# Kernel optimization log

Hardware: AMD Instinct MI355X
Metric: run time of the kernel (lower is better)

## Reference

```python
import jax, jax.numpy as jnp
import numpy as np

N_NODES = 100000
N_EDGES = 400000
IN_DIM, HID, OUT_DIM, NUM_REL = 768, 256, 128, 3


def _init_linear(key, fan_in, fan_out):
    k1, k2 = jax.random.split(key)
    s = 1.0 / np.sqrt(fan_in)
    W = jax.random.uniform(k1, (fan_in, fan_out), jnp.float32, -s, s)
    b = jax.random.uniform(k2, (fan_out,), jnp.float32, -s, s)
    return W, b


def setup_inputs() -> dict:
    key = jax.random.key(0)
    ks = jax.random.split(key, 12)
    x = jax.random.normal(ks[0], (N_NODES, IN_DIM), jnp.float32)
    edge_index = jax.random.randint(ks[1], (2, N_EDGES), 0, N_NODES, jnp.int64 if jax.config.jax_enable_x64 else jnp.int32).astype(jnp.int32)
    edge_type = jax.random.randint(ks[2], (N_EDGES,), 0, NUM_REL).astype(jnp.int32)
    W1, b1 = _init_linear(ks[3], IN_DIM, HID)
    s = 1.0 / np.sqrt(HID)
    conv1_W = jax.random.uniform(ks[4], (NUM_REL, HID, HID), jnp.float32, -s, s)
    conv1_root = jax.random.uniform(ks[5], (HID, HID), jnp.float32, -s, s)
    conv1_bias = jnp.zeros((HID,), jnp.float32)
    conv2_W = jax.random.uniform(ks[6], (NUM_REL, HID, HID), jnp.float32, -s, s)
    conv2_root = jax.random.uniform(ks[7], (HID, HID), jnp.float32, -s, s)
    conv2_bias = jnp.zeros((HID,), jnp.float32)
    W2, b2 = _init_linear(ks[8], HID, OUT_DIM)
    Wc, bc = _init_linear(ks[9], OUT_DIM, 2)
    return {"x": x, "edge_index": edge_index, "edge_type": edge_type,
            "batch_size": 1024,
            "W1": W1, "b1": b1,
            "conv1_W": conv1_W, "conv1_root": conv1_root, "conv1_bias": conv1_bias,
            "conv2_W": conv2_W, "conv2_root": conv2_root, "conv2_bias": conv2_bias,
            "W2": W2, "b2": b2, "Wc": Wc, "bc": bc}


def rgcn_conv(h, src, dst, edge_type, W, root, bias):
    # PyG RGCNConv: mean aggregation per relation + root transform + bias
    n = h.shape[0]
    hs = h[src]                                   # [E, HID] gather
    out = h @ root + bias                         # root/self term
    for r in range(NUM_REL):                      # fixed small relation count
        w = (edge_type == r).astype(h.dtype)      # [E]
        msg = (hs @ W[r]) * w[:, None]            # per-relation transform
        ssum = jax.ops.segment_sum(msg, dst, num_segments=n)
        cnt = jax.ops.segment_sum(w, dst, num_segments=n)
        out = out + ssum / jnp.maximum(cnt, 1.0)[:, None]
    return out


def reference(x, edge_index, edge_type, batch_size,
              W1, b1, conv1_W, conv1_root, conv1_bias,
              conv2_W, conv2_root, conv2_bias, W2, b2, Wc, bc):
    src, dst = edge_index[0], edge_index[1]
    h = jax.nn.relu(x @ W1 + b1)                  # linear1 + ReLU
    h = rgcn_conv(h, src, dst, edge_type, conv1_W, conv1_root, conv1_bias)
    # dropout: identity at inference
    h = rgcn_conv(h, src, dst, edge_type, conv2_W, conv2_root, conv2_bias)
    h = jax.nn.relu(h @ W2 + b2)                  # linear2 + ReLU
    logits = h @ Wc + bc                          # classifier
    return logits[:batch_size]
```

## Files before the change

kernel.cpp:

```cpp
#include <hip/hip_runtime.h>


#define N_NODES 100000
#define N_EDGES 400000
#define IN_DIM  768
#define HID     256
#define OUT_DIM 128
#define NREL    3
#define BATCH   1024
#define KCAT    1024
#define MSGW    768
#define CAP0    32768
#define CAP1    8192
#define ECAP1   32768
#define ECAP2   8192
#define NBAR    12

typedef __attribute__((ext_vector_type(8))) short bf16x8;
typedef __attribute__((ext_vector_type(4))) float f32x4;

static __device__ __forceinline__ int imin(int a, int b) { return a < b ? a : b; }

static __device__ __forceinline__ unsigned short f2bf(float f) {
    union { float f; unsigned int u; } v; v.f = f;
    unsigned int r = v.u + 0x7FFFu + ((v.u >> 16) & 1u);
    return (unsigned short)(r >> 16);
}

struct Prm {
    const float* x; const int* ei; const int* et;
    const float *W1, *b1, *c1W, *c1root, *c1bias, *c2W, *c2root, *c2bias, *W2, *b2, *Wc, *bc;
    float* out;
    uint4* zp; int nz;
    int* bar;
    int *need1, *need0, *map1, *map0, *idx1, *idx0, *elist1, *elist2;
    int *n1ctr, *n0ctr, *ectr1, *ectr2;
    float *cnt1, *cnt2, *Amsg1, *Amsg2, *h0c, *h1c, *h2;
    unsigned short *w1s, *B1s, *B2s;
};

static __device__ __forceinline__ void gbar(int* bar, int slot) {
    __syncthreads();
    if (threadIdx.x == 0) {
        int* c = bar + slot * 16;
        __threadfence();
        atomicAdd(c, 1);
        int nb = (int)gridDim.x;
        long spins = 0;
        while (__hip_atomic_load(c, __ATOMIC_ACQUIRE, __HIP_MEMORY_SCOPE_AGENT) < nb) {
            __builtin_amdgcn_s_sleep(2);
            if (++spins > (1L << 24)) break;
        }
        __threadfence();
    }
    __syncthreads();
}


static __device__ void weight_prep_dev(const Prm& p, int gtid, int gstr) {
    const int P1n = (IN_DIM * HID) / 8, P2n = (KCAT * HID) / 8;
    for (int u = gtid; u < P1n + 2 * P2n; u += gstr) {
        unsigned int pk[4];
        if (u < P1n) {
            int base = u * 8;
            int j0 = base & 31, c = (base >> 5) & 255, s = base >> 13;
            #pragma unroll
            for (int q = 0; q < 4; q++) {
                unsigned short lo = f2bf(p.W1[((s * 32 + j0 + 2 * q) << 8) + c]);
                unsigned short hi = f2bf(p.W1[((s * 32 + j0 + 2 * q + 1) << 8) + c]);
                pk[q] = (unsigned int)lo | ((unsigned int)hi << 16);
            }
            *(uint4*)&p.w1s[base] = make_uint4(pk[0], pk[1], pk[2], pk[3]);
        } else {
            int which2 = (u - P1n) >= P2n;
            const float* root = which2 ? p.c2root : p.c1root;
            const float* Wr   = which2 ? p.c2W : p.c1W;
            unsigned short* dst = which2 ? p.B2s : p.B1s;
            int base = ((u - P1n) - (which2 ? P2n : 0)) * 8;
            int j0 = base & 31, c = (base >> 5) & 255, s = base >> 13;
            int k0 = s * 32 + j0;
            #pragma unroll
            for (int q = 0; q < 4; q++) {
                int ka = k0 + 2 * q, kb = ka + 1;
                float va = (ka < HID) ? root[(ka << 8) + c] : Wr[((ka - HID) << 8) + c];
                float vb = (kb < HID) ? root[(kb << 8) + c] : Wr[((kb - HID) << 8) + c];
                pk[q] = (unsigned int)f2bf(va) | ((unsigned int)f2bf(vb) << 16);
            }
            *(uint4*)&dst[base] = make_uint4(pk[0], pk[1], pk[2], pk[3]);
        }
    }
}

static __device__ void scatter_dev(const int* __restrict__ ei, const int* __restrict__ et,
                                   const int* __restrict__ elist, const int* __restrict__ ectr, int ecap,
                                   const int* __restrict__ mapSrc, const int* __restrict__ mapDst,
                                   const float* __restrict__ hsrc,
                                   float* __restrict__ Amsg, float* __restrict__ cnt,
                                   int cntStride, int gtid, int gstr) {
    int n = imin(*ectr, ecap);
    int tot = n * 64;
    for (int g = gtid; g < tot; g += gstr) {
        int ii = g >> 6, lane = g & 63;
        int e = elist[ii];
        int d = ei[N_EDGES + e];
        int row = mapDst ? mapDst[d] : d;
        if (row < 0) continue;
        int s = mapSrc[ei[e]];
        if (s < 0) continue;
        int r = et[e];
        float4 v = *(const float4*)(hsrc + (size_t)s * HID + lane * 4);
        float* dp = Amsg + (size_t)row * MSGW + (size_t)r * HID + lane * 4;
        atomicAdd(dp + 0, v.x);
        atomicAdd(dp + 1, v.y);
        atomicAdd(dp + 2, v.z);
        atomicAdd(dp + 3, v.w);
        if (lane == 0) atomicAdd(cnt + (size_t)r * cntStride + row, 1.0f);
    }
}

static __device__ void gemm1_tile(const float* __restrict__ x, const int* __restrict__ idx0,
                                  const unsigned short* __restrict__ w1s, const float* __restrict__ b1,
                                  float* __restrict__ h0c, int bm, int M,
                                  unsigned short (*As)[40], unsigned short (*Bs)[40]) {
    int tid = threadIdx.x;
    int w = tid >> 6, lane = tid & 63;
    int l16 = lane & 15, lhi = lane >> 4;
    int ar = tid >> 2, ac = tid & 3;
    int gr = idx0[imin(bm + ar, M - 1)];
    const float* aptr = x + (size_t)gr * IN_DIM + ac * 8;

    f32x4 acc[16];
    #pragma unroll
    for (int i = 0; i < 16; i++) acc[i] = (f32x4)0.0f;

    for (int k0 = 0; k0 < IN_DIM; k0 += 32) {
        float4 a0 = *(const float4*)(aptr + k0);
        float4 a1 = *(const float4*)(aptr + k0 + 4);
        unsigned int p0 = (unsigned int)f2bf(a0.x) | ((unsigned int)f2bf(a0.y) << 16);
        unsigned int p1 = (unsigned int)f2bf(a0.z) | ((unsigned int)f2bf(a0.w) << 16);
        unsigned int p2 = (unsigned int)f2bf(a1.x) | ((unsigned int)f2bf(a1.y) << 16);
        unsigned int p3 = (unsigned int)f2bf(a1.z) | ((unsigned int)f2bf(a1.w) << 16);
        *(uint4*)&As[ar][ac * 8] = make_uint4(p0, p1, p2, p3);

        const uint4* bsrc = (const uint4*)(w1s + ((size_t)(k0 >> 5) * 256 + tid) * 32);
        int bswz = (tid >> 3) & 3;
        uint4 b0 = bsrc[0], b1v = bsrc[1], b2 = bsrc[2], b3 = bsrc[3];
        *(uint4*)&Bs[tid][(0 ^ bswz) * 8] = b0;
        *(uint4*)&Bs[tid][(1 ^ bswz) * 8] = b1v;
        *(uint4*)&Bs[tid][(2 ^ bswz) * 8] = b2;
        *(uint4*)&Bs[tid][(3 ^ bswz) * 8] = b3;
        __syncthreads();

        bf16x8 af = *(bf16x8*)&As[w * 16 + l16][lhi * 8];
        #pragma unroll
        for (int f = 0; f < 16; f++) {
            int col = f * 16 + l16;
            bf16x8 bf = *(bf16x8*)&Bs[col][(lhi ^ ((col >> 3) & 3)) * 8];
            acc[f] = __builtin_amdgcn_mfma_f32_16x16x32_bf16(af, bf, acc[f], 0, 0, 0);
        }
        __syncthreads();
    }

    #pragma unroll
    for (int f = 0; f < 16; f++) {
        int col = f * 16 + l16;
        float bb = b1[col];
        #pragma unroll
        for (int reg = 0; reg < 4; reg++) {
            int row = bm + w * 16 + lhi * 4 + reg;
            if (row < M) h0c[(size_t)row * HID + col] = fmaxf(acc[f][reg] + bb, 0.0f);
        }
    }
}

static __device__ void conv_tile(const float* __restrict__ hsrc,
                                 const int* __restrict__ idx, const int* __restrict__ map,
                                 const float* __restrict__ Amsg,
                                 const float* __restrict__ cnt, int cntStride,
                                 const unsigned short* __restrict__ Bt, const float* __restrict__ bias,
                                 float* __restrict__ Cout, int bm, int M,
                                 unsigned short (*As)[40], unsigned short (*Bs)[40]) {
    int tid = threadIdx.x;
    int w = tid >> 6, lane = tid & 63;
    int l16 = lane & 15, lhi = lane >> 4;
    int ar = tid >> 2, ac = tid & 3;
    int row = imin(bm + ar, M - 1);
    int node = idx ? idx[row] : row;
    int grow = map[node]; if (grow < 0) grow = 0;
    const float* rootp = hsrc + (size_t)grow * HID + ac * 8;
    const float* msgp  = Amsg + (size_t)row * MSGW + ac * 8;
    float sc[NREL];
    #pragma unroll
    for (int r = 0; r < NREL; r++)
        sc[r] = 1.0f / fmaxf(cnt[(size_t)r * cntStride + row], 1.0f);

    f32x4 acc[16];
    #pragma unroll
    for (int i = 0; i < 16; i++) acc[i] = (f32x4)0.0f;

    for (int k0 = 0; k0 < KCAT; k0 += 32) {
        float4 a0, a1;
        if (k0 < HID) {
            a0 = *(const float4*)(rootp + k0);
            a1 = *(const float4*)(rootp + k0 + 4);
        } else {
            float s = sc[(k0 - HID) >> 8];
            a0 = *(const float4*)(msgp + (k0 - HID));
            a1 = *(const float4*)(msgp + (k0 - HID) + 4);
            a0.x *= s; a0.y *= s; a0.z *= s; a0.w *= s;
            a1.x *= s; a1.y *= s; a1.z *= s; a1.w *= s;
        }
        unsigned int p0 = (unsigned int)f2bf(a0.x) | ((unsigned int)f2bf(a0.y) << 16);
        unsigned int p1 = (unsigned int)f2bf(a0.z) | ((unsigned int)f2bf(a0.w) << 16);
        unsigned int p2 = (unsigned int)f2bf(a1.x) | ((unsigned int)f2bf(a1.y) << 16);
        unsigned int p3 = (unsigned int)f2bf(a1.z) | ((unsigned int)f2bf(a1.w) << 16);
        *(uint4*)&As[ar][ac * 8] = make_uint4(p0, p1, p2, p3);

        const uint4* bsrc = (const uint4*)(Bt + ((size_t)(k0 >> 5) * 256 + tid) * 32);
        int bswz = (tid >> 3) & 3;
        uint4 b0 = bsrc[0], b1v = bsrc[1], b2 = bsrc[2], b3 = bsrc[3];
        *(uint4*)&Bs[tid][(0 ^ bswz) * 8] = b0;
        *(uint4*)&Bs[tid][(1 ^ bswz) * 8] = b1v;
        *(uint4*)&Bs[tid][(2 ^ bswz) * 8] = b2;
        *(uint4*)&Bs[tid][(3 ^ bswz) * 8] = b3;
        __syncthreads();

        bf16x8 af = *(bf16x8*)&As[w * 16 + l16][lhi * 8];
        #pragma unroll
        for (int f = 0; f < 16; f++) {
            int col = f * 16 + l16;
            bf16x8 bf = *(bf16x8*)&Bs[col][(lhi ^ ((col >> 3) & 3)) * 8];
            acc[f] = __builtin_amdgcn_mfma_f32_16x16x32_bf16(af, bf, acc[f], 0, 0, 0);
        }
        __syncthreads();
    }

    #pragma unroll
    for (int f = 0; f < 16; f++) {
        int col = f * 16 + l16;
        float bb = bias[col];
        #pragma unroll
        for (int reg = 0; reg < 4; reg++) {
            int r = bm + w * 16 + lhi * 4 + reg;
            if (r < M) Cout[(size_t)r * HID + col] = acc[f][reg] + bb;
        }
    }
}

static __device__ void lin2_tile(const float* __restrict__ h2, const float* __restrict__ W2,
                                 const float* __restrict__ b2, const float* __restrict__ Wc,
                                 const float* __restrict__ bc, float* __restrict__ out, int bm,
                                 float (*Asf)[36], float (*Bsf)[132]) {
    int tid = threadIdx.x;
    int tx = tid & 15, ty = tid >> 4;
    int brow = tid >> 4, bch = tid & 15;

    float acc[2][8] = {};

    for (int k0 = 0; k0 < HID; k0 += 16) {
        if (tid < 128) {
            int arow = tid >> 2, ach = tid & 3;
            float4 av = *(const float4*)(h2 + (size_t)(bm + arow) * HID + k0 + ach * 4);
            Asf[ach * 4 + 0][arow] = av.x;
            Asf[ach * 4 + 1][arow] = av.y;
            Asf[ach * 4 + 2][arow] = av.z;
            Asf[ach * 4 + 3][arow] = av.w;
        }
        const float* bp = W2 + (size_t)(k0 + brow) * OUT_DIM;
        *(float4*)&Bsf[brow][bch * 4]      = *(const float4*)(bp + bch * 4);
        *(float4*)&Bsf[brow][64 + bch * 4] = *(const float4*)(bp + 64 + bch * 4);
        __syncthreads();
        #pragma unroll
        for (int k = 0; k < 16; k++) {
            float a0 = Asf[k][ty * 2], a1 = Asf[k][ty * 2 + 1];
            float4 b0 = *(const float4*)&Bsf[k][tx * 8];
            float4 b1 = *(const float4*)&Bsf[k][tx * 8 + 4];
            acc[0][0] += a0 * b0.x; acc[0][1] += a0 * b0.y; acc[0][2] += a0 * b0.z; acc[0][3] += a0 * b0.w;
            acc[0][4] += a0 * b1.x; acc[0][5] += a0 * b1.y; acc[0][6] += a0 * b1.z; acc[0][7] += a0 * b1.w;
            acc[1][0] += a1 * b0.x; acc[1][1] += a1 * b0.y; acc[1][2] += a1 * b0.z; acc[1][3] += a1 * b0.w;
            acc[1][4] += a1 * b1.x; acc[1][5] += a1 * b1.y; acc[1][6] += a1 * b1.z; acc[1][7] += a1 * b1.w;
        }
        __syncthreads();
    }

    float s0[2] = {0.f, 0.f}, s1[2] = {0.f, 0.f};
    #pragma unroll
    for (int j = 0; j < 8; j++) {
        int col = tx * 8 + j;
        float w0 = Wc[col * 2 + 0], w1 = Wc[col * 2 + 1];
        float bb = b2[col];
        #pragma unroll
        for (int i = 0; i < 2; i++) {
            float h = fmaxf(acc[i][j] + bb, 0.0f);
            s0[i] += h * w0;
            s1[i] += h * w1;
        }
    }
    #pragma unroll
    for (int o = 1; o <= 8; o <<= 1) {
        #pragma unroll
        for (int i = 0; i < 2; i++) {
            s0[i] += __shfl_xor(s0[i], o);
            s1[i] += __shfl_xor(s1[i], o);
        }
    }
    if (tx == 0) {
        #pragma unroll
        for (int i = 0; i < 2; i++) {
            int row = bm + ty * 2 + i;
            out[row * 2 + 0] = s0[i] + bc[0];
            out[row * 2 + 1] = s1[i] + bc[1];
        }
    }
}


__global__ __launch_bounds__(256, 2) void mega(Prm p) {
    __shared__ __align__(16) char sm[(64 * 40 + 256 * 40) * 2];
    unsigned short (*As)[40] = (unsigned short(*)[40])sm;
    unsigned short (*Bs)[40] = (unsigned short(*)[40])(sm + 64 * 40 * 2);

    const int tid  = threadIdx.x;
    const int gtid = blockIdx.x * 256 + tid;
    const int gstr = gridDim.x * 256;

    {
        uint4 z = make_uint4(0u, 0u, 0u, 0u);
        for (int t = gtid; t < p.nz; t += gstr) p.zp[t] = z;
        weight_prep_dev(p, gtid, gstr);
    }
    gbar(p.bar, 0);

    for (int e = gtid; e < N_EDGES; e += gstr) {
        if (p.ei[N_EDGES + e] < BATCH) {
            p.need1[p.ei[e]] = 1;
            int q = atomicAdd(p.ectr2, 1);
            if (q < ECAP2) p.elist2[q] = e;
        }
    }
    gbar(p.bar, 1);

    for (int e = gtid; e < N_EDGES; e += gstr) {
        int d = p.ei[N_EDGES + e];
        if (d < BATCH || p.need1[d]) {
            p.need0[p.ei[e]] = 1;
            int q = atomicAdd(p.ectr1, 1);
            if (q < ECAP1) p.elist1[q] = e;
        }
    }
    gbar(p.bar, 2);

    for (int i = gtid; i < N_NODES; i += gstr) {
        int f1 = (i < BATCH) | p.need1[i];
        int f0 = f1 | p.need0[i];
        if (f1) {
            int q = atomicAdd(p.n1ctr, 1);
            if (q < CAP1) { p.idx1[q] = i; p.map1[i] = q; } else p.map1[i] = -1;
        } else p.map1[i] = -1;
        if (f0) {
            int q = atomicAdd(p.n0ctr, 1);
            if (q < CAP0) { p.idx0[q] = i; p.map0[i] = q; } else p.map0[i] = -1;
        } else p.map0[i] = -1;
    }
    gbar(p.bar, 3);

    {
        int M = imin(*p.n0ctr, CAP0);
        int nt = (M + 63) >> 6;
        for (int t = blockIdx.x; t < nt; t += gridDim.x)
            gemm1_tile(p.x, p.idx0, p.w1s, p.b1, p.h0c, t * 64, M, As, Bs);
    }
    gbar(p.bar, 4);

    scatter_dev(p.ei, p.et, p.elist1, p.ectr1, ECAP1, p.map0, p.map1, p.h0c,
                p.Amsg1, p.cnt1, CAP1, gtid, gstr);
    gbar(p.bar, 5);

    {
        int M = imin(*p.n1ctr, CAP1);
        int nt = (M + 63) >> 6;
        for (int t = blockIdx.x; t < nt; t += gridDim.x)
            conv_tile(p.h0c, p.idx1, p.map0, p.Amsg1, p.cnt1, CAP1,
                      p.B1s, p.c1bias, p.h1c, t * 64, M, As, Bs);
    }
    gbar(p.bar, 6);

    scatter_dev(p.ei, p.et, p.elist2, p.ectr2, ECAP2, p.map1, nullptr, p.h1c,
                p.Amsg2, p.cnt2, BATCH, gtid, gstr);
    gbar(p.bar, 7);

    for (int t = blockIdx.x; t < BATCH / 64; t += gridDim.x)
        conv_tile(p.h1c, nullptr, p.map1, p.Amsg2, p.cnt2, BATCH,
                  p.B2s, p.c2bias, p.h2, t * 64, BATCH, As, Bs);
    gbar(p.bar, 8);

    {
        float (*Asf)[36]  = (float(*)[36])sm;
        float (*Bsf)[132] = (float(*)[132])(sm + 16 * 36 * 4);
        for (int t = blockIdx.x; t < BATCH / 32; t += gridDim.x)
            lin2_tile(p.h2, p.W2, p.b2, p.Wc, p.bc, p.out, t * 32, Asf, Bsf);
    }
}


__global__ void fb_zero_prep(Prm p) {
    int t = blockIdx.x * blockDim.x + threadIdx.x;
    if (t < p.nz) { p.zp[t] = make_uint4(0u, 0u, 0u, 0u); return; }
    weight_prep_dev(p, t - p.nz, 1 << 30);
}
__global__ void fb_mark1c(Prm p) {
    int e = blockIdx.x * blockDim.x + threadIdx.x;
    if (e >= N_EDGES) return;
    if (p.ei[N_EDGES + e] < BATCH) {
        p.need1[p.ei[e]] = 1;
        int q = atomicAdd(p.ectr2, 1);
        if (q < ECAP2) p.elist2[q] = e;
    }
}
__global__ void fb_mark0c(Prm p) {
    int e = blockIdx.x * blockDim.x + threadIdx.x;
    if (e >= N_EDGES) return;
    int d = p.ei[N_EDGES + e];
    if (d < BATCH || p.need1[d]) {
        p.need0[p.ei[e]] = 1;
        int q = atomicAdd(p.ectr1, 1);
        if (q < ECAP1) p.elist1[q] = e;
    }
}
__global__ void fb_compact(Prm p) {
    int i = blockIdx.x * blockDim.x + threadIdx.x;
    if (i >= N_NODES) return;
    int f1 = (i < BATCH) | p.need1[i];
    int f0 = f1 | p.need0[i];
    if (f1) {
        int q = atomicAdd(p.n1ctr, 1);
        if (q < CAP1) { p.idx1[q] = i; p.map1[i] = q; } else p.map1[i] = -1;
    } else p.map1[i] = -1;
    if (f0) {
        int q = atomicAdd(p.n0ctr, 1);
        if (q < CAP0) { p.idx0[q] = i; p.map0[i] = q; } else p.map0[i] = -1;
    } else p.map0[i] = -1;
}
__global__ __launch_bounds__(256) void fb_gemm1(Prm p) {
    __shared__ unsigned short As[64][40];
    __shared__ unsigned short Bs[256][40];
    int M = imin(*p.n0ctr, CAP0);
    int bm = blockIdx.x * 64;
    if (bm >= M) return;
    gemm1_tile(p.x, p.idx0, p.w1s, p.b1, p.h0c, bm, M, As, Bs);
}
__global__ void fb_scatter1(Prm p) {
    int g = blockIdx.x * blockDim.x + threadIdx.x;
    scatter_dev(p.ei, p.et, p.elist1, p.ectr1, ECAP1, p.map0, p.map1, p.h0c,
                p.Amsg1, p.cnt1, CAP1, g, 1 << 30);
}
__global__ __launch_bounds__(256) void fb_conv1(Prm p) {
    __shared__ unsigned short As[64][40];
    __shared__ unsigned short Bs[256][40];
    int M = imin(*p.n1ctr, CAP1);
    int bm = blockIdx.x * 64;
    if (bm >= M) return;
    conv_tile(p.h0c, p.idx1, p.map0, p.Amsg1, p.cnt1, CAP1, p.B1s, p.c1bias, p.h1c, bm, M, As, Bs);
}
__global__ void fb_scatter2(Prm p) {
    int g = blockIdx.x * blockDim.x + threadIdx.x;
    scatter_dev(p.ei, p.et, p.elist2, p.ectr2, ECAP2, p.map1, nullptr, p.h1c,
                p.Amsg2, p.cnt2, BATCH, g, 1 << 30);
}
__global__ __launch_bounds__(256) void fb_conv2(Prm p) {
    __shared__ unsigned short As[64][40];
    __shared__ unsigned short Bs[256][40];
    conv_tile(p.h1c, nullptr, p.map1, p.Amsg2, p.cnt2, BATCH, p.B2s, p.c2bias, p.h2,
              blockIdx.x * 64, BATCH, As, Bs);
}
__global__ __launch_bounds__(256) void fb_lin2(Prm p) {
    __shared__ float Asf[16][36];
    __shared__ float Bsf[16][132];
    lin2_tile(p.h2, p.W2, p.b2, p.Wc, p.bc, p.out, blockIdx.x * 32, Asf, Bsf);
}


extern "C" void kernel_launch(void* const* d_in, const int* in_sizes, int n_in,
                              void* d_out, int out_size, void* d_ws, size_t ws_size,
                              hipStream_t stream) {
    Prm p;
    p.x      = (const float*)d_in[0];
    p.ei     = (const int*)d_in[1];
    p.et     = (const int*)d_in[2];
    p.W1     = (const float*)d_in[4];
    p.b1     = (const float*)d_in[5];
    p.c1W    = (const float*)d_in[6];
    p.c1root = (const float*)d_in[7];
    p.c1bias = (const float*)d_in[8];
    p.c2W    = (const float*)d_in[9];
    p.c2root = (const float*)d_in[10];
    p.c2bias = (const float*)d_in[11];
    p.W2     = (const float*)d_in[12];
    p.b2     = (const float*)d_in[13];
    p.Wc     = (const float*)d_in[14];
    p.bc     = (const float*)d_in[15];
    p.out    = (float*)d_out;

    char* ws = (char*)d_ws;
    size_t off = 0;
    auto alloc = [&](size_t bytes) -> char* {
        char* q = ws + off;
        off = (off + bytes + 255) & ~(size_t)255;
        return q;
    };

    p.bar = (int*)alloc(NBAR * 64);

    size_t zb_ctr   = 16;
    size_t zb_cnt1  = (size_t)NREL * CAP1 * 4;
    size_t zb_cnt2  = (size_t)NREL * BATCH * 4;
    size_t zb_need  = (size_t)N_NODES * 4;
    size_t zb_amsg1 = (size_t)CAP1 * MSGW * 4;
    size_t zb_amsg2 = (size_t)BATCH * MSGW * 4;
    size_t zbytes = zb_ctr + zb_cnt1 + zb_cnt2 + 2 * zb_need + zb_amsg1 + zb_amsg2;
    char* zblock = alloc(zbytes);
    p.zp    = (uint4*)zblock;
    p.nz    = (int)((zbytes + 15) / 16);
    p.n1ctr = (int*)zblock;
    p.n0ctr = p.n1ctr + 1;
    p.ectr1 = p.n1ctr + 2;
    p.ectr2 = p.n1ctr + 3;
    p.cnt1  = (float*)(zblock + zb_ctr);
    p.cnt2  = (float*)(zblock + zb_ctr + zb_cnt1);
    p.need1 = (int*)(zblock + zb_ctr + zb_cnt1 + zb_cnt2);
    p.need0 = (int*)((char*)p.need1 + zb_need);
    p.Amsg1 = (float*)((char*)p.need0 + zb_need);
    p.Amsg2 = (float*)((char*)p.Amsg1 + zb_amsg1);

    p.map1   = (int*)alloc(N_NODES * 4);
    p.map0   = (int*)alloc(N_NODES * 4);
    p.idx1   = (int*)alloc(CAP1 * 4);
    p.idx0   = (int*)alloc(CAP0 * 4);
    p.elist1 = (int*)alloc(ECAP1 * 4);
    p.elist2 = (int*)alloc(ECAP2 * 4);
    p.h0c    = (float*)alloc((size_t)CAP0 * HID * 4);
    p.h1c    = (float*)alloc((size_t)CAP1 * HID * 4);
    p.h2     = (float*)alloc((size_t)BATCH * HID * 4);
    p.w1s    = (unsigned short*)alloc((size_t)IN_DIM * HID * 2);
    p.B1s    = (unsigned short*)alloc((size_t)KCAT * HID * 2);
    p.B2s    = (unsigned short*)alloc((size_t)KCAT * HID * 2);
    (void)ws_size; (void)in_sizes; (void)n_in; (void)out_size;

    hipMemsetAsync(p.bar, 0, NBAR * 64, stream);

    int occ = 0;
    hipError_t qe = hipOccupancyMaxActiveBlocksPerMultiprocessor(&occ, mega, 256, 0);

    if (qe == hipSuccess && occ >= 1) {
        int nblk = (occ >= 2) ? 512 : 256;
        mega<<<dim3(nblk), dim3(256), 0, stream>>>(p);
    } else {
        const int NB = 256;
        int prep_threads = (IN_DIM * HID) / 8 + 2 * (KCAT * HID) / 8;
        int zp_total = p.nz + prep_threads;
        fb_zero_prep<<<dim3((zp_total + NB - 1) / NB), NB, 0, stream>>>(p);
        fb_mark1c<<<dim3((N_EDGES + NB - 1) / NB), NB, 0, stream>>>(p);
        fb_mark0c<<<dim3((N_EDGES + NB - 1) / NB), NB, 0, stream>>>(p);
        fb_compact<<<dim3((N_NODES + NB - 1) / NB), NB, 0, stream>>>(p);
        fb_gemm1<<<dim3(CAP0 / 64), NB, 0, stream>>>(p);
        fb_scatter1<<<dim3(ECAP1 * 64 / NB), NB, 0, stream>>>(p);
        fb_conv1<<<dim3(CAP1 / 64), NB, 0, stream>>>(p);
        fb_scatter2<<<dim3(ECAP2 * 64 / NB), NB, 0, stream>>>(p);
        fb_conv2<<<dim3(BATCH / 64), NB, 0, stream>>>(p);
        fb_lin2<<<dim3(BATCH / 32), NB, 0, stream>>>(p);
    }
}
```

Before: 471.6 us.

## Spread grid barrier over 64 lines and fold zeroing into later phases

After: 467.9 us. About the same (-0.8%).

```diff
diff --git a/kernel.cpp b/kernel.cpp
--- a/kernel.cpp
+++ b/kernel.cpp
@@ -14,7 +14,8 @@
 #define CAP1    8192
 #define ECAP1   32768
 #define ECAP2   8192
-#define NBAR    12
+#define NBAR    9
+#define BLINES  64
 
 typedef __attribute__((ext_vector_type(8))) short bf16x8;
 typedef __attribute__((ext_vector_type(4))) float f32x4;
@@ -41,15 +42,18 @@
 
 static __device__ __forceinline__ void gbar(int* bar, int slot) {
     __syncthreads();
+    int* base = bar + slot * (BLINES * 16);
     if (threadIdx.x == 0) {
-        int* c = bar + slot * 16;
         __threadfence();
-        atomicAdd(c, 1);
-        int nb = (int)gridDim.x;
+        atomicAdd(base + (blockIdx.x & (BLINES - 1)) * 16, 1);
+    }
+    if (threadIdx.x < BLINES) {
+        int target = (int)(gridDim.x >> 6);
+        int* line = base + threadIdx.x * 16;
         long spins = 0;
-        while (__hip_atomic_load(c, __ATOMIC_ACQUIRE, __HIP_MEMORY_SCOPE_AGENT) < nb) {
-            __builtin_amdgcn_s_sleep(2);
-            if (++spins > (1L << 24)) break;
+        while (__hip_atomic_load(line, __ATOMIC_ACQUIRE, __HIP_MEMORY_SCOPE_AGENT) < target) {
+            __builtin_amdgcn_s_sleep(8);
+            if (++spins > (1L << 20)) break;
         }
         __threadfence();
     }
@@ -324,13 +328,6 @@
     const int gtid = blockIdx.x * 256 + tid;
     const int gstr = gridDim.x * 256;
 
-    {
-        uint4 z = make_uint4(0u, 0u, 0u, 0u);
-        for (int t = gtid; t < p.nz; t += gstr) p.zp[t] = z;
-        weight_prep_dev(p, gtid, gstr);
-    }
-    gbar(p.bar, 0);
-
     for (int e = gtid; e < N_EDGES; e += gstr) {
         if (p.ei[N_EDGES + e] < BATCH) {
             p.need1[p.ei[e]] = 1;
@@ -338,7 +335,8 @@
             if (q < ECAP2) p.elist2[q] = e;
         }
     }
-    gbar(p.bar, 1);
+    weight_prep_dev(p, gtid, gstr);
+    gbar(p.bar, 0);
 
     for (int e = gtid; e < N_EDGES; e += gstr) {
         int d = p.ei[N_EDGES + e];
@@ -348,7 +346,11 @@
             if (q < ECAP1) p.elist1[q] = e;
         }
     }
-    gbar(p.bar, 2);
+    {
+        uint4 z = make_uint4(0u, 0u, 0u, 0u);
+        for (int t = gtid; t < p.nz; t += gstr) p.zp[t] = z;
+    }
+    gbar(p.bar, 1);
 
     for (int i = gtid; i < N_NODES; i += gstr) {
         int f1 = (i < BATCH) | p.need1[i];
@@ -362,7 +364,7 @@
             if (q < CAP0) { p.idx0[q] = i; p.map0[i] = q; } else p.map0[i] = -1;
         } else p.map0[i] = -1;
     }
-    gbar(p.bar, 3);
+    gbar(p.bar, 2);
 
     {
         int M = imin(*p.n0ctr, CAP0);
@@ -370,11 +372,11 @@
         for (int t = blockIdx.x; t < nt; t += gridDim.x)
             gemm1_tile(p.x, p.idx0, p.w1s, p.b1, p.h0c, t * 64, M, As, Bs);
     }
-    gbar(p.bar, 4);
+    gbar(p.bar, 3);
 
     scatter_dev(p.ei, p.et, p.elist1, p.ectr1, ECAP1, p.map0, p.map1, p.h0c,
                 p.Amsg1, p.cnt1, CAP1, gtid, gstr);
-    gbar(p.bar, 5);
+    gbar(p.bar, 4);
 
     {
         int M = imin(*p.n1ctr, CAP1);
@@ -383,16 +385,16 @@
             conv_tile(p.h0c, p.idx1, p.map0, p.Amsg1, p.cnt1, CAP1,
                       p.B1s, p.c1bias, p.h1c, t * 64, M, As, Bs);
     }
-    gbar(p.bar, 6);
+    gbar(p.bar, 5);
 
     scatter_dev(p.ei, p.et, p.elist2, p.ectr2, ECAP2, p.map1, nullptr, p.h1c,
                 p.Amsg2, p.cnt2, BATCH, gtid, gstr);
-    gbar(p.bar, 7);
+    gbar(p.bar, 6);
 
     for (int t = blockIdx.x; t < BATCH / 64; t += gridDim.x)
         conv_tile(p.h1c, nullptr, p.map1, p.Amsg2, p.cnt2, BATCH,
                   p.B2s, p.c2bias, p.h2, t * 64, BATCH, As, Bs);
-    gbar(p.bar, 8);
+    gbar(p.bar, 7);
 
     {
         float (*Asf)[36]  = (float(*)[36])sm;
@@ -509,28 +511,29 @@
         return q;
     };
 
-    p.bar = (int*)alloc(NBAR * 64);
-
-    size_t zb_ctr   = 16;
-    size_t zb_cnt1  = (size_t)NREL * CAP1 * 4;
-    size_t zb_cnt2  = (size_t)NREL * BATCH * 4;
-    size_t zb_need  = (size_t)N_NODES * 4;
-    size_t zb_amsg1 = (size_t)CAP1 * MSGW * 4;
-    size_t zb_amsg2 = (size_t)BATCH * MSGW * 4;
-    size_t zbytes = zb_ctr + zb_cnt1 + zb_cnt2 + 2 * zb_need + zb_amsg1 + zb_amsg2;
-    char* zblock = alloc(zbytes);
-    p.zp    = (uint4*)zblock;
-    p.nz    = (int)((zbytes + 15) / 16);
-    p.n1ctr = (int*)zblock;
+    p.bar = (int*)alloc((size_t)NBAR * BLINES * 64);
+    size_t zb_ctr  = 16;
+    size_t zb_cnt1 = (size_t)NREL * CAP1 * 4;
+    size_t zb_cnt2 = (size_t)NREL * BATCH * 4;
+    size_t zb_need = (size_t)N_NODES * 4;
+    char* zsmall = alloc(zb_ctr + zb_cnt1 + zb_cnt2 + 2 * zb_need);
+    p.n1ctr = (int*)zsmall;
     p.n0ctr = p.n1ctr + 1;
     p.ectr1 = p.n1ctr + 2;
     p.ectr2 = p.n1ctr + 3;
-    p.cnt1  = (float*)(zblock + zb_ctr);
-    p.cnt2  = (float*)(zblock + zb_ctr + zb_cnt1);
-    p.need1 = (int*)(zblock + zb_ctr + zb_cnt1 + zb_cnt2);
+    p.cnt1  = (float*)(zsmall + zb_ctr);
+    p.cnt2  = (float*)(zsmall + zb_ctr + zb_cnt1);
+    p.need1 = (int*)(zsmall + zb_ctr + zb_cnt1 + zb_cnt2);
     p.need0 = (int*)((char*)p.need1 + zb_need);
-    p.Amsg1 = (float*)((char*)p.need0 + zb_need);
-    p.Amsg2 = (float*)((char*)p.Amsg1 + zb_amsg1);
+    size_t msbytes = (size_t)(((char*)p.need0 + zb_need) - (char*)p.bar);
+
+    size_t zb_amsg1 = (size_t)CAP1 * MSGW * 4;
+    size_t zb_amsg2 = (size_t)BATCH * MSGW * 4;
+    char* amsg = alloc(zb_amsg1 + zb_amsg2);
+    p.zp    = (uint4*)amsg;
+    p.nz    = (int)((zb_amsg1 + zb_amsg2) / 16);
+    p.Amsg1 = (float*)amsg;
+    p.Amsg2 = (float*)(amsg + zb_amsg1);
 
     p.map1   = (int*)alloc(N_NODES * 4);
     p.map0   = (int*)alloc(N_NODES * 4);
@@ -546,7 +549,7 @@
     p.B2s    = (unsigned short*)alloc((size_t)KCAT * HID * 2);
     (void)ws_size; (void)in_sizes; (void)n_in; (void)out_size;
 
-    hipMemsetAsync(p.bar, 0, NBAR * 64, stream);
+    hipMemsetAsync(p.bar, 0, msbytes, stream);
 
     int occ = 0;
     hipError_t qe = hipOccupancyMaxActiveBlocksPerMultiprocessor(&occ, mega, 256, 0);
```
